# Kernel tuning notes

Measured on AMD Instinct MI355X. Metric: run time of the kernel, lower is better.

Reference implementation:

```python
import jax, jax.numpy as jnp
import numpy as np

RADII = (1.5, 3.0)   # max radii per dilated ring
KS = (32, 64)        # neighbors per ring
OP_C = 64            # per-operator output channels
OUT_C = 256          # agg conv output channels


def setup_inputs() -> dict:
    key = jax.random.key(0)
    k = jax.random.split(key, 8)
    B, N, M, D, C = 4, 8192, 2048, 3, 64
    positions = jax.random.normal(k[0], (B, N, D), dtype=jnp.float32)
    features = jax.random.normal(k[1], (B, N, C), dtype=jnp.float32)
    centers = jax.random.normal(k[2], (B, M, D), dtype=jnp.float32)
    # squared distances in [0, 9) so both rings [1,2.25) and [2.25,9) are hit
    distances = jax.random.uniform(k[3], (B, M, N), dtype=jnp.float32) * 9.0
    W_op0 = jax.random.normal(k[4], (D + C, OP_C), dtype=jnp.float32) * 0.05
    b_op0 = jnp.zeros((OP_C,), dtype=jnp.float32)
    W_op1 = jax.random.normal(k[5], (D + C, OP_C), dtype=jnp.float32) * 0.05
    b_op1 = jnp.zeros((OP_C,), dtype=jnp.float32)
    W_agg = jax.random.normal(k[6], (2 * OP_C, OUT_C), dtype=jnp.float32) * 0.05
    b_agg = jnp.zeros((OUT_C,), dtype=jnp.float32)
    return dict(positions=positions, features=features, centers=centers,
                distances=distances, W_op0=W_op0, b_op0=b_op0,
                W_op1=W_op1, b_op1=b_op1, W_agg=W_agg, b_agg=b_agg)


def reference(positions, features, centers, distances,
              W_op0, b_op0, W_op1, b_op1, W_agg, b_agg):
    B, N, D = positions.shape
    M = centers.shape[1]
    arangeN = jnp.arange(N)
    bidx = jnp.arange(B)[:, None, None]
    min_radius = -1.0  # faithful to source: min_radius**2 == 1 in ring 0
    fs = []
    for max_radius, kk, (W, b) in zip(RADII, KS, ((W_op0, b_op0), (W_op1, b_op1))):
        excluded = (distances >= max_radius ** 2) | (distances < min_radius ** 2)
        idx = jnp.where(excluded, N, arangeN[None, None, :])   # (B,M,N)
        idx = jnp.sort(idx, axis=-1)[:, :, :kk]                # (B,M,k)
        mask = idx != N
        safe = jnp.where(mask, idx, 0)
        pos_g = positions[bidx, safe]                          # (B,M,k,D)
        feat_g = features[bidx, safe]                          # (B,M,k,C)
        rel = pos_g - centers[:, :, None, :]                   # (B,M,k,D)
        h = jax.nn.relu(jnp.concatenate([rel, feat_g], axis=-1) @ W + b)
        h = jnp.where(mask[..., None], h, 0.0)                 # invalid -> zero row
        fs.append(jnp.max(h, axis=2))                          # (B,M,OP_C)
        min_radius = max_radius
    x = jnp.concatenate(fs, axis=-1)                           # (B,M,2*OP_C)
    return jax.nn.relu(x @ W_agg + b_agg)                      # (B,M,OUT_C)
```

## Files before the change

kernel.cpp:

```cpp
#include <hip/hip_runtime.h>
#include <stdint.h>

#define BB 4
#define NN 8192
#define MM 2048
#define CC 64
#define OPC 64
#define OUTC 256
#define K0 32
#define K1 64
#define CPW 4

typedef short bf16x8 __attribute__((ext_vector_type(8)));
typedef float f32x4  __attribute__((ext_vector_type(4)));

__device__ __forceinline__ short f2bf(float f) {
    uint32_t u = __float_as_uint(f);
    u += 0x7FFFu + ((u >> 16) & 1u);
    return (short)(u >> 16);
}

__device__ __forceinline__ uint32_t cvt_pk_bf16(float a, float b) {
    uint32_t r;
    asm("v_cvt_pk_bf16_f32 %0, %1, %2" : "=v"(r) : "v"(a), "v"(b));
    return r;
}

__device__ __forceinline__ bf16x8 pack8(float4 a, float4 b) {
    union { uint4 u; bf16x8 v; } r;
    r.u.x = cvt_pk_bf16(a.x, a.y);
    r.u.y = cvt_pk_bf16(a.z, a.w);
    r.u.z = cvt_pk_bf16(b.x, b.y);
    r.u.w = cvt_pk_bf16(b.z, b.w);
    return r.v;
}

__global__ __launch_bounds__(256, 2) void op_kernel(
    const float* __restrict__ positions, const float* __restrict__ features,
    const float* __restrict__ centers,   const float* __restrict__ distances,
    const float* __restrict__ W0, const float* __restrict__ b0,
    const float* __restrict__ W1, const float* __restrict__ b1,
    const float* __restrict__ Wagg, const float* __restrict__ bagg,
    float* __restrict__ out)
{
    __shared__ float s_x[4][CPW][128];
    __shared__ int s_idx0[4][K0];
    __shared__ int s_idx1[4][K1];

    const int w    = threadIdx.x >> 6;
    const int lane = threadIdx.x & 63;
    const int quad = lane >> 4;
    const int l15  = lane & 15;
    const int gw   = blockIdx.x * 4 + w;

    bf16x8 bfr0[3][4], bfr1[3][4];
#pragma unroll
    for (int kc = 0; kc < 3; ++kc) {
#pragma unroll
        for (int nt = 0; nt < 4; ++nt) {
            const int n = nt * 16 + l15;
            bf16x8 v0, v1;
#pragma unroll
            for (int j = 0; j < 8; ++j) {
                int k = kc * 32 + quad * 8 + j;
                float a0 = 0.f, a1 = 0.f;
                if (k < 64)      { a0 = W0[(3 + k) * OPC + n];  a1 = W1[(3 + k) * OPC + n]; }
                else if (k < 67) { a0 = W0[(k - 64) * OPC + n]; a1 = W1[(k - 64) * OPC + n]; }
                v0[j] = f2bf(a0); v1[j] = f2bf(a1);
            }
            bfr0[kc][nt] = v0; bfr1[kc][nt] = v1;
        }
    }
    float bias0v[4], bias1v[4];
#pragma unroll
    for (int nt = 0; nt < 4; ++nt) {
        bias0v[nt] = b0[nt * 16 + l15];
        bias1v[nt] = b1[nt * 16 + l15];
    }
    const unsigned long long lt = (1ull << lane) - 1ull;
    const bf16x8 zf = {0, 0, 0, 0, 0, 0, 0, 0};

    for (int i = 0; i < CPW; ++i) {
        const int bm = gw * CPW + i;
        const int b  = bm >> 11;

        const float* drow = distances + (size_t)bm * NN;
        int cnt0 = 0, cnt1 = 0;
        for (int base = 0; base < NN; base += 512) {
            if (cnt0 >= K0 && cnt1 >= K1) break;
            float dv[8];
#pragma unroll
            for (int u = 0; u < 8; ++u) dv[u] = drow[base + u * 64 + lane];
#pragma unroll
            for (int u = 0; u < 8; ++u) {
                float d = dv[u];
                bool p0 = (d >= 1.0f)  && (d < 2.25f);
                bool p1 = (d >= 2.25f) && (d < 9.0f);
                unsigned long long m0 = __ballot(p0);
                unsigned long long m1 = __ballot(p1);
                if (cnt0 < K0) {
                    int pos = cnt0 + __popcll(m0 & lt);
                    if (p0 && pos < K0) s_idx0[w][pos] = base + u * 64 + lane;
                    cnt0 += __popcll(m0);
                }
                if (cnt1 < K1) {
                    int pos = cnt1 + __popcll(m1 & lt);
                    if (p1 && pos < K1) s_idx1[w][pos] = base + u * 64 + lane;
                    cnt1 += __popcll(m1);
                }
            }
        }
        cnt0 = min(cnt0, K0);
        cnt1 = min(cnt1, K1);

        const float cx = centers[(size_t)bm * 3 + 0];
        const float cy = centers[(size_t)bm * 3 + 1];
        const float cz = centers[(size_t)bm * 3 + 2];

        {
            float cm[4] = {0.f, 0.f, 0.f, 0.f};
#pragma unroll
            for (int mt = 0; mt < 4; ++mt) {
                const int r = mt * 16 + l15;
                const int n = (r < cnt1) ? s_idx1[w][r] : 0;
                const float4* fb = (const float4*)(features + (size_t)((size_t)b * NN + n) * CC);
                float4 a0 = fb[quad * 2],     a1 = fb[quad * 2 + 1];
                float4 a2 = fb[8 + quad * 2], a3 = fb[8 + quad * 2 + 1];
                const float* pp = positions + (size_t)((size_t)b * NN + n) * 3;
                float rx = pp[0] - cx, ry = pp[1] - cy, rz = pp[2] - cz;
                bf16x8 af0 = pack8(a0, a1);
                bf16x8 af1 = pack8(a2, a3);
                union { uint4 u; bf16x8 v; } r2;
                r2.u.x = cvt_pk_bf16(rx, ry);
                r2.u.y = cvt_pk_bf16(rz, 0.0f);
                r2.u.z = 0u; r2.u.w = 0u;
                bf16x8 af2 = (quad == 0) ? r2.v : zf;

                f32x4 acc[4];
#pragma unroll
                for (int nt = 0; nt < 4; ++nt)
                    acc[nt] = (f32x4){bias1v[nt], bias1v[nt], bias1v[nt], bias1v[nt]};
#pragma unroll
                for (int nt = 0; nt < 4; ++nt)
                    acc[nt] = __builtin_amdgcn_mfma_f32_16x16x32_bf16(af0, bfr1[0][nt], acc[nt], 0, 0, 0);
#pragma unroll
                for (int nt = 0; nt < 4; ++nt)
                    acc[nt] = __builtin_amdgcn_mfma_f32_16x16x32_bf16(af1, bfr1[1][nt], acc[nt], 0, 0, 0);
#pragma unroll
                for (int nt = 0; nt < 4; ++nt)
                    acc[nt] = __builtin_amdgcn_mfma_f32_16x16x32_bf16(af2, bfr1[2][nt], acc[nt], 0, 0, 0);
#pragma unroll
                for (int nt = 0; nt < 4; ++nt)
#pragma unroll
                    for (int rr = 0; rr < 4; ++rr) {
                        int m = mt * 16 + quad * 4 + rr;
                        float v = (m < cnt1) ? fmaxf(acc[nt][rr], 0.f) : 0.f;
                        cm[nt] = fmaxf(cm[nt], v);
                    }
            }
#pragma unroll
            for (int nt = 0; nt < 4; ++nt) {
                cm[nt] = fmaxf(cm[nt], __shfl_xor(cm[nt], 16, 64));
                cm[nt] = fmaxf(cm[nt], __shfl_xor(cm[nt], 32, 64));
            }
            float f = (quad == 0) ? cm[0] : (quad == 1) ? cm[1]
                    : (quad == 2) ? cm[2] : cm[3];
            s_x[w][i][64 + lane] = f;
        }

        {
            float cm[4] = {0.f, 0.f, 0.f, 0.f};
#pragma unroll
            for (int mt = 0; mt < 2; ++mt) {
                const int r = mt * 16 + l15;
                const int n = (r < cnt0) ? s_idx0[w][r] : 0;
                const float4* fb = (const float4*)(features + (size_t)((size_t)b * NN + n) * CC);
                float4 a0 = fb[quad * 2],     a1 = fb[quad * 2 + 1];
                float4 a2 = fb[8 + quad * 2], a3 = fb[8 + quad * 2 + 1];
                const float* pp = positions + (size_t)((size_t)b * NN + n) * 3;
                float rx = pp[0] - cx, ry = pp[1] - cy, rz = pp[2] - cz;
                bf16x8 af0 = pack8(a0, a1);
                bf16x8 af1 = pack8(a2, a3);
                union { uint4 u; bf16x8 v; } r2;
                r2.u.x = cvt_pk_bf16(rx, ry);
                r2.u.y = cvt_pk_bf16(rz, 0.0f);
                r2.u.z = 0u; r2.u.w = 0u;
                bf16x8 af2 = (quad == 0) ? r2.v : zf;

                f32x4 acc[4];
#pragma unroll
                for (int nt = 0; nt < 4; ++nt)
                    acc[nt] = (f32x4){bias0v[nt], bias0v[nt], bias0v[nt], bias0v[nt]};
#pragma unroll
                for (int nt = 0; nt < 4; ++nt)
                    acc[nt] = __builtin_amdgcn_mfma_f32_16x16x32_bf16(af0, bfr0[0][nt], acc[nt], 0, 0, 0);
#pragma unroll
                for (int nt = 0; nt < 4; ++nt)
                    acc[nt] = __builtin_amdgcn_mfma_f32_16x16x32_bf16(af1, bfr0[1][nt], acc[nt], 0, 0, 0);
#pragma unroll
                for (int nt = 0; nt < 4; ++nt)
                    acc[nt] = __builtin_amdgcn_mfma_f32_16x16x32_bf16(af2, bfr0[2][nt], acc[nt], 0, 0, 0);
#pragma unroll
                for (int nt = 0; nt < 4; ++nt)
#pragma unroll
                    for (int rr = 0; rr < 4; ++rr) {
                        int m = mt * 16 + quad * 4 + rr;
                        float v = (m < cnt0) ? fmaxf(acc[nt][rr], 0.f) : 0.f;
                        cm[nt] = fmaxf(cm[nt], v);
                    }
            }
#pragma unroll
            for (int nt = 0; nt < 4; ++nt) {
                cm[nt] = fmaxf(cm[nt], __shfl_xor(cm[nt], 16, 64));
                cm[nt] = fmaxf(cm[nt], __shfl_xor(cm[nt], 32, 64));
            }
            float f = (quad == 0) ? cm[0] : (quad == 1) ? cm[1]
                    : (quad == 2) ? cm[2] : cm[3];
            s_x[w][i][lane] = f;
        }
    }

    {
        float4 bias4 = ((const float4*)bagg)[lane];
        f32x4 acc[CPW];
#pragma unroll
        for (int i = 0; i < CPW; ++i)
            acc[i] = (f32x4){bias4.x, bias4.y, bias4.z, bias4.w};

#pragma unroll 2
        for (int c4 = 0; c4 < 32; ++c4) {
            float4 xv[CPW];
#pragma unroll
            for (int i = 0; i < CPW; ++i)
                xv[i] = *(const float4*)&s_x[w][i][c4 * 4];
#pragma unroll
            for (int u = 0; u < 4; ++u) {
                const int c = c4 * 4 + u;
                float4 wv = *(const float4*)(Wagg + (size_t)c * OUTC + lane * 4);
#pragma unroll
                for (int i = 0; i < CPW; ++i) {
                    const float xc = (u == 0) ? xv[i].x : (u == 1) ? xv[i].y
                                   : (u == 2) ? xv[i].z : xv[i].w;
                    acc[i][0] = fmaf(xc, wv.x, acc[i][0]);
                    acc[i][1] = fmaf(xc, wv.y, acc[i][1]);
                    acc[i][2] = fmaf(xc, wv.z, acc[i][2]);
                    acc[i][3] = fmaf(xc, wv.w, acc[i][3]);
                }
            }
        }
#pragma unroll
        for (int i = 0; i < CPW; ++i) {
            float4 o = make_float4(fmaxf(acc[i][0], 0.f), fmaxf(acc[i][1], 0.f),
                                   fmaxf(acc[i][2], 0.f), fmaxf(acc[i][3], 0.f));
            *(float4*)(out + (size_t)(gw * CPW + i) * OUTC + lane * 4) = o;
        }
    }
}

extern "C" void kernel_launch(void* const* d_in, const int* in_sizes, int n_in,
                              void* d_out, int out_size, void* d_ws, size_t ws_size,
                              hipStream_t stream) {
    const float* positions = (const float*)d_in[0];
    const float* features  = (const float*)d_in[1];
    const float* centers   = (const float*)d_in[2];
    const float* distances = (const float*)d_in[3];
    const float* W0        = (const float*)d_in[4];
    const float* b0        = (const float*)d_in[5];
    const float* W1        = (const float*)d_in[6];
    const float* b1        = (const float*)d_in[7];
    const float* Wagg      = (const float*)d_in[8];
    const float* bagg      = (const float*)d_in[9];
    float* out = (float*)d_out;
    (void)d_ws; (void)ws_size;

    op_kernel<<<512, 256, 0, stream>>>(positions, features, centers, distances,
                                       W0, b0, W1, b1, Wagg, bagg, out);
}
```

Baseline: 353.6 us.

## Prefetch next center's first distance chunk and restructure agg GEMM per block

```diff
diff --git a/kernel.cpp b/kernel.cpp
--- a/kernel.cpp
+++ b/kernel.cpp
@@ -33,6 +33,30 @@
     r.u.z = cvt_pk_bf16(b.x, b.y);
     r.u.w = cvt_pk_bf16(b.z, b.w);
     return r.v;
+}
+
+__device__ __forceinline__ void process8(const float* dv, int base, int lane,
+                                         unsigned long long lt,
+                                         int* s0, int* s1,
+                                         int& cnt0, int& cnt1) {
+#pragma unroll
+    for (int u = 0; u < 8; ++u) {
+        float d = dv[u];
+        bool p0 = (d >= 1.0f)  && (d < 2.25f);
+        bool p1 = (d >= 2.25f) && (d < 9.0f);
+        unsigned long long m0 = __ballot(p0);
+        unsigned long long m1 = __ballot(p1);
+        if (cnt0 < K0) {
+            int pos = cnt0 + __popcll(m0 & lt);
+            if (p0 && pos < K0) s0[pos] = base + u * 64 + lane;
+            cnt0 += __popcll(m0);
+        }
+        if (cnt1 < K1) {
+            int pos = cnt1 + __popcll(m1 & lt);
+            if (p1 && pos < K1) s1[pos] = base + u * 64 + lane;
+            cnt1 += __popcll(m1);
+        }
+    }
 }
 
 __global__ __launch_bounds__(256, 2) void op_kernel(
@@ -80,42 +104,45 @@
     const unsigned long long lt = (1ull << lane) - 1ull;
     const bf16x8 zf = {0, 0, 0, 0, 0, 0, 0, 0};
 
+    float dvp[8];
+    float cxp, cyp, czp;
+    {
+        const float* drow0 = distances + (size_t)(gw * CPW) * NN;
+#pragma unroll
+        for (int u = 0; u < 8; ++u) dvp[u] = drow0[u * 64 + lane];
+        cxp = centers[(size_t)(gw * CPW) * 3 + 0];
+        cyp = centers[(size_t)(gw * CPW) * 3 + 1];
+        czp = centers[(size_t)(gw * CPW) * 3 + 2];
+    }
+
     for (int i = 0; i < CPW; ++i) {
         const int bm = gw * CPW + i;
         const int b  = bm >> 11;
-
-        const float* drow = distances + (size_t)bm * NN;
+        const float cx = cxp, cy = cyp, cz = czp;
+
         int cnt0 = 0, cnt1 = 0;
-        for (int base = 0; base < NN; base += 512) {
-            if (cnt0 >= K0 && cnt1 >= K1) break;
-            float dv[8];
-#pragma unroll
-            for (int u = 0; u < 8; ++u) dv[u] = drow[base + u * 64 + lane];
-#pragma unroll
-            for (int u = 0; u < 8; ++u) {
-                float d = dv[u];
-                bool p0 = (d >= 1.0f)  && (d < 2.25f);
-                bool p1 = (d >= 2.25f) && (d < 9.0f);
-                unsigned long long m0 = __ballot(p0);
-                unsigned long long m1 = __ballot(p1);
-                if (cnt0 < K0) {
-                    int pos = cnt0 + __popcll(m0 & lt);
-                    if (p0 && pos < K0) s_idx0[w][pos] = base + u * 64 + lane;
-                    cnt0 += __popcll(m0);
-                }
-                if (cnt1 < K1) {
-                    int pos = cnt1 + __popcll(m1 & lt);
-                    if (p1 && pos < K1) s_idx1[w][pos] = base + u * 64 + lane;
-                    cnt1 += __popcll(m1);
-                }
+        process8(dvp, 0, lane, lt, s_idx0[w], s_idx1[w], cnt0, cnt1);
+        if (cnt0 < K0 || cnt1 < K1) {
+            const float* drow = distances + (size_t)bm * NN;
+            for (int base = 512; base < NN; base += 512) {
+                if (cnt0 >= K0 && cnt1 >= K1) break;
+                float dv[8];
+#pragma unroll
+                for (int u = 0; u < 8; ++u) dv[u] = drow[base + u * 64 + lane];
+                process8(dv, base, lane, lt, s_idx0[w], s_idx1[w], cnt0, cnt1);
             }
         }
         cnt0 = min(cnt0, K0);
         cnt1 = min(cnt1, K1);
 
-        const float cx = centers[(size_t)bm * 3 + 0];
-        const float cy = centers[(size_t)bm * 3 + 1];
-        const float cz = centers[(size_t)bm * 3 + 2];
+        if (i + 1 < CPW) {
+            const float* drn = distances + (size_t)(bm + 1) * NN;
+#pragma unroll
+            for (int u = 0; u < 8; ++u) dvp[u] = drn[u * 64 + lane];
+            cxp = centers[(size_t)(bm + 1) * 3 + 0];
+            cyp = centers[(size_t)(bm + 1) * 3 + 1];
+            czp = centers[(size_t)(bm + 1) * 3 + 2];
+        }
 
         {
             float cm[4] = {0.f, 0.f, 0.f, 0.f};
@@ -220,40 +247,35 @@
         }
     }
 
+    __syncthreads();
     {
-        float4 bias4 = ((const float4*)bagg)[lane];
-        f32x4 acc[CPW];
-#pragma unroll
-        for (int i = 0; i < CPW; ++i)
-            acc[i] = (f32x4){bias4.x, bias4.y, bias4.z, bias4.w};
-
-#pragma unroll 2
+        const int j   = threadIdx.x;
+        const int bm0 = blockIdx.x * 16;
+        float acc[16];
+        const float bj = bagg[j];
+#pragma unroll
+        for (int ci = 0; ci < 16; ++ci) acc[ci] = bj;
+
         for (int c4 = 0; c4 < 32; ++c4) {
-            float4 xv[CPW];
-#pragma unroll
-            for (int i = 0; i < CPW; ++i)
-                xv[i] = *(const float4*)&s_x[w][i][c4 * 4];
-#pragma unroll
-            for (int u = 0; u < 4; ++u) {
-                const int c = c4 * 4 + u;
-                float4 wv = *(const float4*)(Wagg + (size_t)c * OUTC + lane * 4);
-#pragma unroll
-                for (int i = 0; i < CPW; ++i) {
-                    const float xc = (u == 0) ? xv[i].x : (u == 1) ? xv[i].y
-                                   : (u == 2) ? xv[i].z : xv[i].w;
-                    acc[i][0] = fmaf(xc, wv.x, acc[i][0]);
-                    acc[i][1] = fmaf(xc, wv.y, acc[i][1]);
-                    acc[i][2] = fmaf(xc, wv.z, acc[i][2]);
-                    acc[i][3] = fmaf(xc, wv.w, acc[i][3]);
-                }
-            }
-        }
-#pragma unroll
-        for (int i = 0; i < CPW; ++i) {
-            float4 o = make_float4(fmaxf(acc[i][0], 0.f), fmaxf(acc[i][1], 0.f),
-                                   fmaxf(acc[i][2], 0.f), fmaxf(acc[i][3], 0.f));
-            *(float4*)(out + (size_t)(gw * CPW + i) * OUTC + lane * 4) = o;
-        }
+            float4 xq[16];
+#pragma unroll
+            for (int ci = 0; ci < 16; ++ci)
+                xq[ci] = *(const float4*)&s_x[ci >> 2][ci & 3][c4 * 4];
+            const float wv0 = Wagg[(size_t)(c4 * 4 + 0) * OUTC + j];
+            const float wv1 = Wagg[(size_t)(c4 * 4 + 1) * OUTC + j];
+            const float wv2 = Wagg[(size_t)(c4 * 4 + 2) * OUTC + j];
+            const float wv3 = Wagg[(size_t)(c4 * 4 + 3) * OUTC + j];
+#pragma unroll
+            for (int ci = 0; ci < 16; ++ci) {
+                acc[ci] = fmaf(xq[ci].x, wv0, acc[ci]);
+                acc[ci] = fmaf(xq[ci].y, wv1, acc[ci]);
+                acc[ci] = fmaf(xq[ci].z, wv2, acc[ci]);
+                acc[ci] = fmaf(xq[ci].w, wv3, acc[ci]);
+            }
+        }
+#pragma unroll
+        for (int ci = 0; ci < 16; ++ci)
+            out[(size_t)(bm0 + ci) * OUTC + j] = fmaxf(acc[ci], 0.f);
     }
 }
 
```

Measured after the change: 359.9 us. About the same (+1.8%).
